# Kernel tuning notes

Measured on AMD Instinct MI355X. Metric: run time of the kernel, lower is better.

## Reference

```python
import jax, jax.numpy as jnp
import numpy as np

N_IN = 50000
N_OUT = 50000
DEG = 16
E = N_OUT * DEG
C = 64
F = 64


def cartesian_to_spherical(cart, extents):
    # cart: [E,3]
    r_plane_2 = cart[..., 0] ** 2 + cart[..., 1] ** 2
    r_2 = r_plane_2 + cart[..., 2] ** 2
    r_safe = jnp.maximum(jnp.sqrt(r_2), 1e-10)
    cos_phi = cart[..., 2] / r_safe
    r_plane_safe = jnp.maximum(jnp.sqrt(r_plane_2), 1e-10)
    sin_theta = cart[..., 1] / r_plane_safe
    cos_theta = cart[..., 0] / r_plane_safe
    r_normalized = r_safe / extents
    return jnp.stack([r_normalized, cos_phi, sin_theta, cos_theta], axis=-1)  # [E,4]


def setup_inputs() -> dict:
    key = jax.random.key(0)
    k1, k2, k3, k4, k5 = jax.random.split(key, 5)
    input_features = jax.random.normal(k1, (N_IN, C), dtype=jnp.float32)
    input_positions = jax.random.uniform(k2, (N_IN, 3), dtype=jnp.float32)
    output_positions = jax.random.uniform(k3, (N_OUT, 3), dtype=jnp.float32)
    extents = jnp.ones((1,), dtype=jnp.float32)
    kernel = jax.random.normal(k4, (4, C, F), dtype=jnp.float32) * (1.0 / np.sqrt(C))
    bias = jnp.zeros((F,), dtype=jnp.float32)
    neighbors_index = jax.random.randint(k5, (E,), 0, N_IN, dtype=jnp.int32)
    neighbors_row_splits = (DEG * jnp.arange(N_OUT + 1)).astype(jnp.int32)
    return {
        "input_features": input_features,
        "input_positions": input_positions,
        "output_positions": output_positions,
        "extents": extents,
        "kernel": kernel,
        "bias": bias,
        "neighbors_index": neighbors_index,
        "neighbors_row_splits": neighbors_row_splits,
    }


def reference(input_features, input_positions, output_positions, extents,
              kernel, bias, neighbors_index, neighbors_row_splits):
    n_out = output_positions.shape[0]
    n_edges = neighbors_index.shape[0]
    counts = neighbors_row_splits[1:] - neighbors_row_splits[:-1]  # [N_out]
    # segment id of each edge (which output point it belongs to)
    seg_ids = jnp.repeat(jnp.arange(n_out), counts, total_repeat_length=n_edges)
    expanded_query = output_positions[seg_ids]                     # [E,3]
    difference = input_positions[neighbors_index] - expanded_query  # [E,3]
    sph = cartesian_to_spherical(difference, extents)              # [E,4]
    neighbors_feats = input_features[neighbors_index]              # [E,C]
    # contract features with kernel over C first -> [E,4,F] (avoids [E,C,F])
    tmp = jnp.einsum('ec,scf->esf', neighbors_feats, kernel)
    out_edge = jnp.einsum('es,esf->ef', sph, tmp)                  # [E,F]
    out_features = jax.ops.segment_sum(out_edge, seg_ids, num_segments=n_out)
    out_features = out_features + bias
    return out_features
```

## Files before the change

kernel.cpp:

```cpp
#include <hip/hip_runtime.h>

typedef unsigned short u16;
typedef __attribute__((ext_vector_type(8))) short bf16x8;
typedef __attribute__((ext_vector_type(8))) unsigned short u16x8;
typedef __attribute__((ext_vector_type(4))) float f32x4;

#define BLOCK 128

__device__ __forceinline__ float bf2f(u16 u) {
    union { unsigned i; float f; } v; v.i = (unsigned)u << 16; return v.f;
}
__device__ __forceinline__ u16 f2bf(float f) {
    union { float f; unsigned u; } v; v.f = f;
    unsigned r = v.u + 0x7fff + ((v.u >> 16) & 1);
    return (u16)(r >> 16);
}

__global__ __launch_bounds__(256)
void prep_all(const float* __restrict__ feats, const float* __restrict__ kmat,
              u16* __restrict__ fbf, u16* __restrict__ kbg, int n8) {
    const int id = blockIdx.x * 256 + threadIdx.x;
    if (id < n8) {
        const float4 a = ((const float4*)feats)[2 * id];
        const float4 b = ((const float4*)feats)[2 * id + 1];
        union { u16 h[8]; int4 v; } p;
        p.h[0] = f2bf(a.x); p.h[1] = f2bf(a.y); p.h[2] = f2bf(a.z); p.h[3] = f2bf(a.w);
        p.h[4] = f2bf(b.x); p.h[5] = f2bf(b.y); p.h[6] = f2bf(b.z); p.h[7] = f2bf(b.w);
        ((int4*)fbf)[id] = p.v;
    }
    if (id < 16384) {
        const int k = id >> 6, n = id & 63;
        const int kstep = k >> 5, quad = (k >> 3) & 3, j = k & 7;
        const int ntile = n >> 4, lanep = (quad << 4) | (n & 15);
        kbg[((((ntile << 3) | kstep) << 6) | lanep) * 8 + j] = f2bf(kmat[id]);
    }
}

template<bool WS>
__global__ __launch_bounds__(BLOCK)
void sphconv_tile(const float* __restrict__ featsf,
                  const u16* __restrict__ fbf,
                  const u16* __restrict__ kbg,
                  const float* __restrict__ in_pos,
                  const float* __restrict__ out_pos,
                  const float* __restrict__ extents,
                  const float* __restrict__ kmat,
                  const float* __restrict__ bias,
                  const int* __restrict__ nidx,
                  const int* __restrict__ rsplits,
                  float* __restrict__ out,
                  int n_out, int n_edges)
{
    __shared__ _Float16 sphT[16][16][4];
    __shared__ int      idxT[16][16];
    __shared__ __align__(16) float redT[4][64][4];

    const int tid = threadIdx.x;
    const int kh  = tid >> 6;
    const int lane = tid & 63;
    const int m = lane & 15, quad = lane >> 4;
    const int obase = blockIdx.x << 4;

    const float inv_ext = __fdividef(1.f, extents[0]);

    #pragma unroll
    for (int u = 0; u < 2; ++u) {
        const int slot = (u << 7) | tid;
        const int mm = slot >> 4, t = slot & 15;
        const int o  = obase + mm;
        const int oc = min(o, n_out - 1);
        const int e0 = rsplits[oc], e1 = rsplits[oc + 1];
        const int e  = e0 + t;
        const bool v = (o < n_out) && (e < e1);
        const int id = nidx[min(e, n_edges - 1)];
        const float dx = in_pos[id * 3 + 0] - out_pos[oc * 3 + 0];
        const float dy = in_pos[id * 3 + 1] - out_pos[oc * 3 + 1];
        const float dz = in_pos[id * 3 + 2] - out_pos[oc * 3 + 2];
        const float rp2 = dx * dx + dy * dy;
        const float r2  = rp2 + dz * dz;
        const float rs  = fmaxf(sqrtf(r2), 1e-10f);
        const float rp  = fmaxf(sqrtf(rp2), 1e-10f);
        const float ir  = __fdividef(1.f, rs);
        const float irp = __fdividef(1.f, rp);
        union { _Float16 hh[4]; short4 s4; } pk;
        pk.hh[0] = (_Float16)(v ? rs * inv_ext : 0.f);
        pk.hh[1] = (_Float16)(v ? dz * ir      : 0.f);
        pk.hh[2] = (_Float16)(v ? dy * irp     : 0.f);
        pk.hh[3] = (_Float16)(v ? dx * irp     : 0.f);
        idxT[t][mm] = id;
        *(short4*)&sphT[t][mm][0] = pk.s4;
    }
    __syncthreads();

    float acc[4][8];
    #pragma unroll
    for (int s = 0; s < 4; ++s)
        #pragma unroll
        for (int j = 0; j < 8; ++j) acc[s][j] = 0.f;

    #pragma unroll 4
    for (int t = 0; t < 16; ++t) {
        const int idx = idxT[t][m];
        union { short4 s4; _Float16 hh[4]; } up;
        up.s4 = *(const short4*)&sphT[t][m][0];
        float fv[8];
        if constexpr (WS) {
            const u16x8 f0 = *(const u16x8*)(fbf + (idx << 6) + (kh << 5) + (quad << 3));
            #pragma unroll
            for (int j = 0; j < 8; ++j) fv[j] = bf2f(f0[j]);
        } else {
            const float* fr = featsf + (idx << 6) + (kh << 5) + (quad << 3);
            const float4 a0 = *(const float4*)fr;
            const float4 a1 = *(const float4*)(fr + 4);
            fv[0] = a0.x; fv[1] = a0.y; fv[2] = a0.z; fv[3] = a0.w;
            fv[4] = a1.x; fv[5] = a1.y; fv[6] = a1.z; fv[7] = a1.w;
        }
        #pragma unroll
        for (int s = 0; s < 4; ++s) {
            const float w = (float)up.hh[s];
            #pragma unroll
            for (int j = 0; j < 8; ++j)
                acc[s][j] = fmaf(w, fv[j], acc[s][j]);
        }
    }

    bf16x8 afr[4];
    #pragma unroll
    for (int s = 0; s < 4; ++s) {
        union { u16 hh[8]; bf16x8 v; } p;
        #pragma unroll
        for (int j = 0; j < 8; ++j) p.hh[j] = f2bf(acc[s][j]);
        afr[s] = p.v;
    }

    f32x4 C[4] = {{0,0,0,0},{0,0,0,0},{0,0,0,0},{0,0,0,0}};
    #pragma unroll
    for (int nt = 0; nt < 4; ++nt) {
        bf16x8 b[4];
        #pragma unroll
        for (int s = 0; s < 4; ++s) {
            const int ks = (s << 1) | kh;
            if constexpr (WS) {
                b[s] = *(const bf16x8*)(kbg + ((((nt << 3) | ks) << 6) | lane) * 8);
            } else {
                union { u16 hh[8]; bf16x8 v; } p;
                #pragma unroll
                for (int j = 0; j < 8; ++j) {
                    const int k = (ks << 5) | (quad << 3) | j;
                    const int n = (nt << 4) | m;
                    p.hh[j] = f2bf(kmat[k * 64 + n]);
                }
                b[s] = p.v;
            }
        }
        #pragma unroll
        for (int s = 0; s < 4; ++s)
            C[nt] = __builtin_amdgcn_mfma_f32_16x16x32_bf16(afr[s], b[s], C[nt], 0, 0, 0);
    }

    if (kh == 1) {
        #pragma unroll
        for (int nt = 0; nt < 4; ++nt)
            *(f32x4*)&redT[nt][lane][0] = C[nt];
    }
    __syncthreads();
    if (kh == 0) {
        #pragma unroll
        for (int nt = 0; nt < 4; ++nt) {
            const f32x4 P = *(const f32x4*)&redT[nt][lane][0];
            const int f = (nt << 4) | m;
            const float bv = bias[f];
            #pragma unroll
            for (int r = 0; r < 4; ++r) {
                const int oo = obase + (quad << 2) + r;
                if (oo < n_out) out[(oo << 6) | f] = C[nt][r] + P[r] + bv;
            }
        }
    }
}

extern "C" void kernel_launch(void* const* d_in, const int* in_sizes, int n_in,
                              void* d_out, int out_size, void* d_ws, size_t ws_size,
                              hipStream_t stream) {
    const float* feats   = (const float*)d_in[0];
    const float* in_pos  = (const float*)d_in[1];
    const float* out_pos = (const float*)d_in[2];
    const float* extents = (const float*)d_in[3];
    const float* kmat    = (const float*)d_in[4];
    const float* bias    = (const float*)d_in[5];
    const int*   nidx    = (const int*)d_in[6];
    const int*   rsplits = (const int*)d_in[7];
    const int n_out   = in_sizes[7] - 1;
    const int n_edges = in_sizes[6];
    const int ntiles  = (n_out + 15) >> 4;

    const size_t fbf_bytes = (size_t)in_sizes[0] * 2;
    const size_t need = fbf_bytes + 32768;
    if (ws_size >= need && (in_sizes[0] & 7) == 0) {
        u16* fbf = (u16*)d_ws;
        u16* kbg = (u16*)((char*)d_ws + fbf_bytes);
        const int n8 = in_sizes[0] / 8;
        const int pmax = n8 > 16384 ? n8 : 16384;
        prep_all<<<(pmax + 255) / 256, 256, 0, stream>>>(feats, kmat, fbf, kbg, n8);
        sphconv_tile<true><<<ntiles, BLOCK, 0, stream>>>(
            feats, fbf, kbg, in_pos, out_pos, extents, kmat, bias, nidx, rsplits,
            (float*)d_out, n_out, n_edges);
    } else {
        sphconv_tile<false><<<ntiles, BLOCK, 0, stream>>>(
            feats, nullptr, nullptr, in_pos, out_pos, extents, kmat, bias, nidx, rsplits,
            (float*)d_out, n_out, n_edges);
    }
}
```

Baseline: 107.5 us.

## Process two tiles per block and prefetch second tile's gathers during first compute

Each block now handles two consecutive 16-output tiles instead of one, halving the grid. The neighbor-index and position loads for the second tile are issued before the first tile's feature-gather and MFMA work, and their spherical math runs afterwards. The aim is to hide gather latency behind compute. In exchange the grid is half as large, which lowers the number of resident waves available to hide latency. Register pressure also rises from holding the prefetched values.

```diff
diff --git a/kernel.cpp b/kernel.cpp
--- a/kernel.cpp
+++ b/kernel.cpp
@@ -38,7 +38,7 @@
 
 template<bool WS>
 __global__ __launch_bounds__(BLOCK)
-void sphconv_tile(const float* __restrict__ featsf,
+void sphconv_pipe(const float* __restrict__ featsf,
                   const u16* __restrict__ fbf,
                   const u16* __restrict__ kbg,
                   const float* __restrict__ in_pos,
@@ -49,134 +49,175 @@
                   const int* __restrict__ nidx,
                   const int* __restrict__ rsplits,
                   float* __restrict__ out,
-                  int n_out, int n_edges)
+                  int n_out, int ntiles, int n_edges)
 {
     __shared__ _Float16 sphT[16][16][4];
     __shared__ int      idxT[16][16];
     __shared__ __align__(16) float redT[4][64][4];
 
-    const int tid = threadIdx.x;
-    const int kh  = tid >> 6;
+    const int tid  = threadIdx.x;
+    const int kh   = tid >> 6;
     const int lane = tid & 63;
     const int m = lane & 15, quad = lane >> 4;
-    const int obase = blockIdx.x << 4;
-
     const float inv_ext = __fdividef(1.f, extents[0]);
 
-    #pragma unroll
-    for (int u = 0; u < 2; ++u) {
-        const int slot = (u << 7) | tid;
-        const int mm = slot >> 4, t = slot & 15;
-        const int o  = obase + mm;
-        const int oc = min(o, n_out - 1);
-        const int e0 = rsplits[oc], e1 = rsplits[oc + 1];
-        const int e  = e0 + t;
-        const bool v = (o < n_out) && (e < e1);
-        const int id = nidx[min(e, n_edges - 1)];
-        const float dx = in_pos[id * 3 + 0] - out_pos[oc * 3 + 0];
-        const float dy = in_pos[id * 3 + 1] - out_pos[oc * 3 + 1];
-        const float dz = in_pos[id * 3 + 2] - out_pos[oc * 3 + 2];
-        const float rp2 = dx * dx + dy * dy;
-        const float r2  = rp2 + dz * dz;
-        const float rs  = fmaxf(sqrtf(r2), 1e-10f);
-        const float rp  = fmaxf(sqrtf(rp2), 1e-10f);
-        const float ir  = __fdividef(1.f, rs);
-        const float irp = __fdividef(1.f, rp);
-        union { _Float16 hh[4]; short4 s4; } pk;
-        pk.hh[0] = (_Float16)(v ? rs * inv_ext : 0.f);
-        pk.hh[1] = (_Float16)(v ? dz * ir      : 0.f);
-        pk.hh[2] = (_Float16)(v ? dy * irp     : 0.f);
-        pk.hh[3] = (_Float16)(v ? dx * irp     : 0.f);
-        idxT[t][mm] = id;
-        *(short4*)&sphT[t][mm][0] = pk.s4;
-    }
+    const int t0 = blockIdx.x * 2;
+    const int t1 = t0 + 1;
+
+    int   a_id[2]; bool a_v[2];
+    float a_px[2], a_py[2], a_pz[2], a_qx[2], a_qy[2], a_qz[2];
+
+    auto a1_issue = [&](int tile) {
+        const int obase = min(tile, ntiles - 1) << 4;
+        #pragma unroll
+        for (int u = 0; u < 2; ++u) {
+            const int slot = (u << 7) | tid;
+            const int mm = slot >> 4, t = slot & 15;
+            const int o  = obase + mm;
+            const int oc = min(o, n_out - 1);
+            const int e0 = rsplits[oc], e1 = rsplits[oc + 1];
+            const int e  = e0 + t;
+            a_v[u] = (o < n_out) && (e < e1);
+            const int id = nidx[min(e, n_edges - 1)];
+            a_id[u] = id;
+            a_px[u] = in_pos[id * 3 + 0];
+            a_py[u] = in_pos[id * 3 + 1];
+            a_pz[u] = in_pos[id * 3 + 2];
+            a_qx[u] = out_pos[oc * 3 + 0];
+            a_qy[u] = out_pos[oc * 3 + 1];
+            a_qz[u] = out_pos[oc * 3 + 2];
+        }
+    };
+
+    auto a1_math = [&]() {
+        #pragma unroll
+        for (int u = 0; u < 2; ++u) {
+            const int slot = (u << 7) | tid;
+            const int mm = slot >> 4, t = slot & 15;
+            const float dx = a_px[u] - a_qx[u];
+            const float dy = a_py[u] - a_qy[u];
+            const float dz = a_pz[u] - a_qz[u];
+            const float rp2 = dx * dx + dy * dy;
+            const float r2  = rp2 + dz * dz;
+            const float rs  = fmaxf(sqrtf(r2), 1e-10f);
+            const float rp  = fmaxf(sqrtf(rp2), 1e-10f);
+            const float ir  = __fdividef(1.f, rs);
+            const float irp = __fdividef(1.f, rp);
+            union { _Float16 hh[4]; short4 s4; } pk;
+            pk.hh[0] = (_Float16)(a_v[u] ? rs * inv_ext : 0.f);
+            pk.hh[1] = (_Float16)(a_v[u] ? dz * ir      : 0.f);
+            pk.hh[2] = (_Float16)(a_v[u] ? dy * irp     : 0.f);
+            pk.hh[3] = (_Float16)(a_v[u] ? dx * irp     : 0.f);
+            idxT[t][mm] = a_id[u];
+            *(short4*)&sphT[t][mm][0] = pk.s4;
+        }
+    };
+
+    auto compute = [&](f32x4* C) {
+        float acc[4][8];
+        #pragma unroll
+        for (int s = 0; s < 4; ++s)
+            #pragma unroll
+            for (int j = 0; j < 8; ++j) acc[s][j] = 0.f;
+
+        #pragma unroll 4
+        for (int t = 0; t < 16; ++t) {
+            const int idx = idxT[t][m];
+            union { short4 s4; _Float16 hh[4]; } up;
+            up.s4 = *(const short4*)&sphT[t][m][0];
+            float fv[8];
+            if constexpr (WS) {
+                const u16x8 f0 = *(const u16x8*)(fbf + (idx << 6) + (kh << 5) + (quad << 3));
+                #pragma unroll
+                for (int j = 0; j < 8; ++j) fv[j] = bf2f(f0[j]);
+            } else {
+                const float* fr = featsf + (idx << 6) + (kh << 5) + (quad << 3);
+                const float4 a0 = *(const float4*)fr;
+                const float4 a1 = *(const float4*)(fr + 4);
+                fv[0] = a0.x; fv[1] = a0.y; fv[2] = a0.z; fv[3] = a0.w;
+                fv[4] = a1.x; fv[5] = a1.y; fv[6] = a1.z; fv[7] = a1.w;
+            }
+            #pragma unroll
+            for (int s = 0; s < 4; ++s) {
+                const float w = (float)up.hh[s];
+                #pragma unroll
+                for (int j = 0; j < 8; ++j)
+                    acc[s][j] = fmaf(w, fv[j], acc[s][j]);
+            }
+        }
+
+        bf16x8 afr[4];
+        #pragma unroll
+        for (int s = 0; s < 4; ++s) {
+            union { u16 hh[8]; bf16x8 v; } p;
+            #pragma unroll
+            for (int j = 0; j < 8; ++j) p.hh[j] = f2bf(acc[s][j]);
+            afr[s] = p.v;
+        }
+
+        #pragma unroll
+        for (int nt = 0; nt < 4; ++nt) {
+            C[nt] = (f32x4){0.f, 0.f, 0.f, 0.f};
+            bf16x8 b[4];
+            #pragma unroll
+            for (int s = 0; s < 4; ++s) {
+                const int ks = (s << 1) | kh;
+                if constexpr (WS) {
+                    b[s] = *(const bf16x8*)(kbg + ((((nt << 3) | ks) << 6) | lane) * 8);
+                } else {
+                    union { u16 hh[8]; bf16x8 v; } p;
+                    #pragma unroll
+                    for (int j = 0; j < 8; ++j) {
+                        const int k = (ks << 5) | (quad << 3) | j;
+                        const int n = (nt << 4) | m;
+                        p.hh[j] = f2bf(kmat[k * 64 + n]);
+                    }
+                    b[s] = p.v;
+                }
+            }
+            #pragma unroll
+            for (int s = 0; s < 4; ++s)
+                C[nt] = __builtin_amdgcn_mfma_f32_16x16x32_bf16(afr[s], b[s], C[nt], 0, 0, 0);
+        }
+    };
+
+    auto reduce_store = [&](const f32x4* C, int tile) {
+        if (kh == 1) {
+            #pragma unroll
+            for (int nt = 0; nt < 4; ++nt)
+                *(f32x4*)&redT[nt][lane][0] = C[nt];
+        }
+        __syncthreads();
+        if (kh == 0 && tile < ntiles) {
+            const int obase = tile << 4;
+            #pragma unroll
+            for (int nt = 0; nt < 4; ++nt) {
+                const f32x4 P = *(const f32x4*)&redT[nt][lane][0];
+                const int f = (nt << 4) | m;
+                const float bv = bias[f];
+                #pragma unroll
+                for (int r = 0; r < 4; ++r) {
+                    const int oo = obase + (quad << 2) + r;
+                    if (oo < n_out) out[(oo << 6) | f] = C[nt][r] + P[r] + bv;
+                }
+            }
+        }
+    };
+
+    a1_issue(t0);
+    a1_math();
     __syncthreads();
 
-    float acc[4][8];
-    #pragma unroll
-    for (int s = 0; s < 4; ++s)
-        #pragma unroll
-        for (int j = 0; j < 8; ++j) acc[s][j] = 0.f;
-
-    #pragma unroll 4
-    for (int t = 0; t < 16; ++t) {
-        const int idx = idxT[t][m];
-        union { short4 s4; _Float16 hh[4]; } up;
-        up.s4 = *(const short4*)&sphT[t][m][0];
-        float fv[8];
-        if constexpr (WS) {
-            const u16x8 f0 = *(const u16x8*)(fbf + (idx << 6) + (kh << 5) + (quad << 3));
-            #pragma unroll
-            for (int j = 0; j < 8; ++j) fv[j] = bf2f(f0[j]);
-        } else {
-            const float* fr = featsf + (idx << 6) + (kh << 5) + (quad << 3);
-            const float4 a0 = *(const float4*)fr;
-            const float4 a1 = *(const float4*)(fr + 4);
-            fv[0] = a0.x; fv[1] = a0.y; fv[2] = a0.z; fv[3] = a0.w;
-            fv[4] = a1.x; fv[5] = a1.y; fv[6] = a1.z; fv[7] = a1.w;
-        }
-        #pragma unroll
-        for (int s = 0; s < 4; ++s) {
-            const float w = (float)up.hh[s];
-            #pragma unroll
-            for (int j = 0; j < 8; ++j)
-                acc[s][j] = fmaf(w, fv[j], acc[s][j]);
-        }
-    }
-
-    bf16x8 afr[4];
-    #pragma unroll
-    for (int s = 0; s < 4; ++s) {
-        union { u16 hh[8]; bf16x8 v; } p;
-        #pragma unroll
-        for (int j = 0; j < 8; ++j) p.hh[j] = f2bf(acc[s][j]);
-        afr[s] = p.v;
-    }
-
-    f32x4 C[4] = {{0,0,0,0},{0,0,0,0},{0,0,0,0},{0,0,0,0}};
-    #pragma unroll
-    for (int nt = 0; nt < 4; ++nt) {
-        bf16x8 b[4];
-        #pragma unroll
-        for (int s = 0; s < 4; ++s) {
-            const int ks = (s << 1) | kh;
-            if constexpr (WS) {
-                b[s] = *(const bf16x8*)(kbg + ((((nt << 3) | ks) << 6) | lane) * 8);
-            } else {
-                union { u16 hh[8]; bf16x8 v; } p;
-                #pragma unroll
-                for (int j = 0; j < 8; ++j) {
-                    const int k = (ks << 5) | (quad << 3) | j;
-                    const int n = (nt << 4) | m;
-                    p.hh[j] = f2bf(kmat[k * 64 + n]);
-                }
-                b[s] = p.v;
-            }
-        }
-        #pragma unroll
-        for (int s = 0; s < 4; ++s)
-            C[nt] = __builtin_amdgcn_mfma_f32_16x16x32_bf16(afr[s], b[s], C[nt], 0, 0, 0);
-    }
-
-    if (kh == 1) {
-        #pragma unroll
-        for (int nt = 0; nt < 4; ++nt)
-            *(f32x4*)&redT[nt][lane][0] = C[nt];
-    }
+    a1_issue(t1);
+    f32x4 C0[4];
+    compute(C0);
+    reduce_store(C0, t0);
+    a1_math();
     __syncthreads();
-    if (kh == 0) {
-        #pragma unroll
-        for (int nt = 0; nt < 4; ++nt) {
-            const f32x4 P = *(const f32x4*)&redT[nt][lane][0];
-            const int f = (nt << 4) | m;
-            const float bv = bias[f];
-            #pragma unroll
-            for (int r = 0; r < 4; ++r) {
-                const int oo = obase + (quad << 2) + r;
-                if (oo < n_out) out[(oo << 6) | f] = C[nt][r] + P[r] + bv;
-            }
-        }
-    }
+
+    f32x4 C1[4];
+    compute(C1);
+    reduce_store(C1, t1);
 }
 
 extern "C" void kernel_launch(void* const* d_in, const int* in_sizes, int n_in,
@@ -193,6 +234,7 @@
     const int n_out   = in_sizes[7] - 1;
     const int n_edges = in_sizes[6];
     const int ntiles  = (n_out + 15) >> 4;
+    const int grid    = (ntiles + 1) >> 1;
 
     const size_t fbf_bytes = (size_t)in_sizes[0] * 2;
     const size_t need = fbf_bytes + 32768;
@@ -202,12 +244,12 @@
         const int n8 = in_sizes[0] / 8;
         const int pmax = n8 > 16384 ? n8 : 16384;
         prep_all<<<(pmax + 255) / 256, 256, 0, stream>>>(feats, kmat, fbf, kbg, n8);
-        sphconv_tile<true><<<ntiles, BLOCK, 0, stream>>>(
+        sphconv_pipe<true><<<grid, BLOCK, 0, stream>>>(
             feats, fbf, kbg, in_pos, out_pos, extents, kmat, bias, nidx, rsplits,
-            (float*)d_out, n_out, n_edges);
+            (float*)d_out, n_out, ntiles, n_edges);
     } else {
-        sphconv_tile<false><<<ntiles, BLOCK, 0, stream>>>(
+        sphconv_pipe<false><<<grid, BLOCK, 0, stream>>>(
             feats, nullptr, nullptr, in_pos, out_pos, extents, kmat, bias, nidx, rsplits,
-            (float*)d_out, n_out, n_edges);
+            (float*)d_out, n_out, ntiles, n_edges);
     }
 }
```

After: 115.0 us. +7.0%, slower.
